# Kernel optimization log

Hardware: AMD Instinct MI355X
Metric: run time of the kernel (lower is better)

The kernel has to match this reference:

```python
import jax, jax.numpy as jnp
import numpy as np

# Static module configuration (matches init_kwargs)
B, C_IN, H, W = 128, 64, 32, 32
C_OUT = 128
K = 3
PAD = 1
STRIDE = 1
OUT_H = (H + 2 * PAD - K) // STRIDE + 1  # 32
OUT_W = (W + 2 * PAD - K) // STRIDE + 1  # 32
L = OUT_H * OUT_W                        # 1024
IN_FEAT = C_IN * K * K                   # 576


def setup_inputs() -> dict:
    key = jax.random.key(0)
    k1, k2, k3 = jax.random.split(key, 3)
    x = jax.random.normal(k1, (B, C_IN, H, W), dtype=jnp.float32)
    # kaiming-uniform-ish scale: 1/sqrt(fan_in)
    bound = 1.0 / np.sqrt(IN_FEAT)
    weight = jax.random.uniform(k2, (L, IN_FEAT, C_OUT), dtype=jnp.float32,
                                minval=-bound, maxval=bound)
    bias = jax.random.uniform(k3, (L, C_OUT), dtype=jnp.float32,
                              minval=-bound, maxval=bound)
    return {"x": x, "weight": weight, "bias": bias}


def _unfold(x):
    """torch.nn.Unfold equivalent: returns (B, L, C*K*K), channel-major feature order."""
    xp = jnp.pad(x, ((0, 0), (0, 0), (PAD, PAD), (PAD, PAD)))
    cols = []
    for i in range(K):
        for j in range(K):
            cols.append(xp[:, :, i:i + OUT_H * STRIDE:STRIDE,
                               j:j + OUT_W * STRIDE:STRIDE])
    # (B, C, K*K, out_h, out_w) -> feature index = c*K*K + i*K + j (torch unfold order)
    p = jnp.stack(cols, axis=2)
    p = p.reshape(x.shape[0], C_IN * K * K, L)
    return p.transpose(0, 2, 1)  # (B, L, in_feat)


def reference(x, weight, bias):
    patches = _unfold(x)                                  # (B, L, in_feat)
    out = jnp.einsum('bli,lio->blo', patches, weight)     # per-location matmul
    out = out + bias[None]                                # (B, L, out_ch)
    out = out.transpose(0, 2, 1).reshape(x.shape[0], C_OUT, OUT_H, OUT_W)
    out = jax.nn.relu(out)
    # MaxPool2d(2, 2)
    Bn = out.shape[0]
    out = out.reshape(Bn, C_OUT, OUT_H // 2, 2, OUT_W // 2, 2).max(axis=(3, 5))
    return out
```

## Files before the change

kernel.cpp:

```cpp
#include <hip/hip_runtime.h>

#define BB   128
#define CI   64
#define HH   32
#define WW   32
#define CO   128
#define IF   576
#define OW   32
#define XH   34
#define XW   34
#define XP_CB    (CI*BB)
#define XP_ELEMS ((size_t)XH*XW*CI*BB)
#define BK   32
#define NIT  72
#define LDK  40
#define COB  64

using short8 = __attribute__((ext_vector_type(8))) short;
using bf16x4 = __attribute__((ext_vector_type(4))) short;
using f32x4  = __attribute__((ext_vector_type(4))) float;

__device__ __forceinline__ unsigned short f2bf(float f) {
  union { float f; unsigned int u; } v; v.f = f;
  unsigned int u = v.u;
  u = (u + 0x7FFFu + ((u >> 16) & 1u)) >> 16;
  return (unsigned short)u;
}

__global__ __launch_bounds__(256) void transpose_x(
    const float* __restrict__ x, unsigned short* __restrict__ xp) {
  const int c = blockIdx.x >> 5;
  const int h = blockIdx.x & 31;
  __shared__ __align__(16) unsigned short tile[32][136];
  const int t = threadIdx.x;
  const int w = t & 31, b0 = t >> 5;
#pragma unroll
  for (int p = 0; p < 16; ++p) {
    int b = b0 + p * 8;
    float v = x[(((size_t)b * CI + c) * HH + h) * WW + w];
    tile[w][b] = f2bf(v);
  }
  __syncthreads();
  const int w2 = t >> 3;
  const int bb = (t & 7) * 16;
  const unsigned short* src = &tile[w2][bb];
  unsigned short* dst = xp + ((size_t)(h + 1) * XW + (w2 + 1)) * XP_CB + c * BB + bb;
  *(uint4*)(dst)     = *(const uint4*)(src);
  *(uint4*)(dst + 8) = *(const uint4*)(src + 8);
}

__global__ __launch_bounds__(512, 4) void local_gemm_pool(
    const float* __restrict__ Wt, const float* __restrict__ bias,
    const unsigned short* __restrict__ xp, float* __restrict__ out) {
  __shared__ __align__(16) unsigned short Asl[2][BB][LDK];
  __shared__ __align__(16) unsigned short Bsl[2][COB][LDK];
  __shared__ int offs[IF];

  const int tid  = threadIdx.x;
  const int lane = tid & 63;
  const int wave = tid >> 6;

  for (int kk = tid; kk < IF; kk += 512) {
    int c = kk / 9, r = kk % 9, di = r / 3, dj = r % 3;
    offs[kk] = ((di * XW + dj) * CI + c) * BB;
  }

  const int bidx = blockIdx.x;
  const int x8 = bidx & 7, j = bidx >> 3;
  const int coh = j & 1;
  const int pw  = (j >> 1) & 15;
  const int ph  = 2 * x8 + (j >> 5);
  const int co0 = coh * COB;

  const int sa = tid & 127;
  const int ka = tid >> 7;
  const int sb = tid & 63;
  const int kb = tid >> 6;

  const int r16 = lane & 15;
  const int q8  = (lane >> 4) * 8;
  const int m0  = (wave >> 2) * 64;
  const int n0  = (wave & 3) * 16;

  f32x4 acc[4] = {};
  f32x4 rmx[4] = {};

  float          breg0[4], breg1[4];
  unsigned short areg0[8], areg1[8];

  __syncthreads();

  auto issue = [&](int it, float* br, unsigned short* ar) {
    const int loc = it / 18, kc = it % 18, k0 = kc * BK;
    const int oh = 2 * ph + (loc >> 1), ow = 2 * pw + (loc & 1);
    const int l  = oh * OW + ow;
    const float* wp = Wt + ((size_t)l * IF + (k0 + kb * 4)) * CO + co0 + sb;
#pragma unroll
    for (int i = 0; i < 4; ++i) br[i] = wp[(size_t)i * CO];
    const int base = (oh * XW + ow) * XP_CB + sa;
#pragma unroll
    for (int i = 0; i < 8; ++i) ar[i] = xp[base + offs[k0 + ka * 8 + i]];
  };

  auto writeLds = [&](int it, const float* br, const unsigned short* ar) {
    const int bufI = it & 1;
    bf16x4 vb;
#pragma unroll
    for (int i = 0; i < 4; ++i) vb[i] = (short)f2bf(br[i]);
    *(bf16x4*)&Bsl[bufI][sb][kb * 4] = vb;
    short8 va;
#pragma unroll
    for (int i = 0; i < 8; ++i) va[i] = (short)ar[i];
    *(short8*)&Asl[bufI][sa][ka * 8] = va;
  };

  auto computeChunk = [&](int it) {
    const int bufI = it & 1;
    short8 af[4], bf;
#pragma unroll
    for (int tm = 0; tm < 4; ++tm)
      af[tm] = *(const short8*)&Asl[bufI][m0 + tm * 16 + r16][q8];
    bf = *(const short8*)&Bsl[bufI][n0 + r16][q8];
#pragma unroll
    for (int tm = 0; tm < 4; ++tm)
      acc[tm] = __builtin_amdgcn_mfma_f32_16x16x32_bf16(af[tm], bf, acc[tm], 0, 0, 0);
  };

  auto finishLoc = [&](int loc) {
    const int oh = 2 * ph + (loc >> 1), ow = 2 * pw + (loc & 1);
    const int l  = oh * OW + ow;
    const float bv = bias[l * CO + co0 + n0 + r16];
#pragma unroll
    for (int tm = 0; tm < 4; ++tm)
#pragma unroll
      for (int e = 0; e < 4; ++e) {
        float v = acc[tm][e] + bv;
        v = v > 0.f ? v : 0.f;
        rmx[tm][e] = fmaxf(rmx[tm][e], v);
        acc[tm][e] = 0.f;
      }
  };

  issue(0, breg0, areg0);
  issue(1, breg1, areg1);
  writeLds(0, breg0, areg0);
  __syncthreads();

  for (int it2 = 0; it2 < NIT; it2 += 2) {
    if (it2 + 2 < NIT) issue(it2 + 2, breg0, areg0);
    computeChunk(it2);
    writeLds(it2 + 1, breg1, areg1);
    __syncthreads();
    const int ito = it2 + 1;
    if (ito + 2 < NIT) issue(ito + 2, breg1, areg1);
    computeChunk(ito);
    if (ito + 1 < NIT) writeLds(ito + 1, breg0, areg0);
    if (ito % 18 == 17) finishLoc(ito / 18);
    __syncthreads();
  }

  float* op = out + (ph * 16 + pw);
  const int col = co0 + n0 + r16;
#pragma unroll
  for (int tm = 0; tm < 4; ++tm)
#pragma unroll
    for (int e = 0; e < 4; ++e) {
      const int row = m0 + tm * 16 + (lane >> 4) * 4 + e;
      op[((size_t)row * CO + col) * 256] = rmx[tm][e];
    }
}

extern "C" void kernel_launch(void* const* d_in, const int* in_sizes, int n_in,
                              void* d_out, int out_size, void* d_ws, size_t ws_size,
                              hipStream_t stream) {
  (void)in_sizes; (void)n_in; (void)out_size; (void)ws_size;
  const float* x  = (const float*)d_in[0];
  const float* w  = (const float*)d_in[1];
  const float* bs = (const float*)d_in[2];
  float* out = (float*)d_out;
  unsigned short* xp = (unsigned short*)d_ws;

  hipMemsetAsync(xp, 0, XP_ELEMS * sizeof(unsigned short), stream);
  transpose_x<<<dim3(CI * HH), dim3(256), 0, stream>>>(x, xp);
  local_gemm_pool<<<dim3(512), dim3(512), 0, stream>>>(w, bs, xp, out);
}
```

Measured before the change: 460.8 us.

## Reorder K loop by kernel tap, fuse halo zeroing, use packed bf16 convert

The reduction is reordered so each 32-wide chunk covers one (di,dj) tap and 32 channels. Activation gathers become strided loads without the LDS offset table, and weight rows are read with a stride of 9. The full memset of the padded buffer is dropped; the transpose kernel now zeroes only the halo border. Weight conversion to bf16 uses the packed v_cvt_pk_bf16_f32 instruction, which is round-to-nearest and should match the old manual rounding. Weight reads are now strided across feature rows, which may hurt coalescing per issue.

```diff
diff --git a/kernel.cpp b/kernel.cpp
--- a/kernel.cpp
+++ b/kernel.cpp
@@ -17,7 +17,6 @@
 #define COB  64
 
 using short8 = __attribute__((ext_vector_type(8))) short;
-using bf16x4 = __attribute__((ext_vector_type(4))) short;
 using f32x4  = __attribute__((ext_vector_type(4))) float;
 
 __device__ __forceinline__ unsigned short f2bf(float f) {
@@ -25,6 +24,12 @@
   unsigned int u = v.u;
   u = (u + 0x7FFFu + ((u >> 16) & 1u)) >> 16;
   return (unsigned short)u;
+}
+
+__device__ __forceinline__ unsigned int cvt_pk_bf16(float lo, float hi) {
+  unsigned int r;
+  asm("v_cvt_pk_bf16_f32 %0, %1, %2" : "=v"(r) : "v"(lo), "v"(hi));
+  return r;
 }
 
 __global__ __launch_bounds__(256) void transpose_x(
@@ -47,6 +52,17 @@
   unsigned short* dst = xp + ((size_t)(h + 1) * XW + (w2 + 1)) * XP_CB + c * BB + bb;
   *(uint4*)(dst)     = *(const uint4*)(src);
   *(uint4*)(dst + 8) = *(const uint4*)(src + 8);
+
+  if (blockIdx.x < 132) {
+    int s = blockIdx.x, hh, wh;
+    if (s < 34)      { hh = 0;  wh = s; }
+    else if (s < 68) { hh = 33; wh = s - 34; }
+    else             { int k = s - 68; hh = 1 + (k >> 1); wh = (k & 1) * 33; }
+    uint4 z; z.x = z.y = z.z = z.w = 0u;
+    uint4* p = (uint4*)(xp + ((size_t)hh * XW + wh) * XP_CB) + t;
+#pragma unroll
+    for (int q = 0; q < 4; ++q) p[q * 256] = z;
+  }
 }
 
 __global__ __launch_bounds__(512, 4) void local_gemm_pool(
@@ -54,16 +70,10 @@
     const unsigned short* __restrict__ xp, float* __restrict__ out) {
   __shared__ __align__(16) unsigned short Asl[2][BB][LDK];
   __shared__ __align__(16) unsigned short Bsl[2][COB][LDK];
-  __shared__ int offs[IF];
 
   const int tid  = threadIdx.x;
   const int lane = tid & 63;
   const int wave = tid >> 6;
-
-  for (int kk = tid; kk < IF; kk += 512) {
-    int c = kk / 9, r = kk % 9, di = r / 3, dj = r % 3;
-    offs[kk] = ((di * XW + dj) * CI + c) * BB;
-  }
 
   const int bidx = blockIdx.x;
   const int x8 = bidx & 7, j = bidx >> 3;
@@ -88,26 +98,28 @@
   float          breg0[4], breg1[4];
   unsigned short areg0[8], areg1[8];
 
-  __syncthreads();
-
   auto issue = [&](int it, float* br, unsigned short* ar) {
-    const int loc = it / 18, kc = it % 18, k0 = kc * BK;
+    const int loc = it / 18, kc = it % 18;
+    const int r = kc >> 1, c0 = (kc & 1) * 32;
+    const int di = r / 3, dj = r % 3;
     const int oh = 2 * ph + (loc >> 1), ow = 2 * pw + (loc & 1);
     const int l  = oh * OW + ow;
-    const float* wp = Wt + ((size_t)l * IF + (k0 + kb * 4)) * CO + co0 + sb;
+    const float* wp = Wt + ((size_t)l * IF + (size_t)(c0 + kb * 4) * 9 + r) * CO
+                         + co0 + sb;
 #pragma unroll
-    for (int i = 0; i < 4; ++i) br[i] = wp[(size_t)i * CO];
-    const int base = (oh * XW + ow) * XP_CB + sa;
+    for (int i = 0; i < 4; ++i) br[i] = wp[(size_t)i * 9 * CO];
+    const unsigned short* ap = xp + ((size_t)(oh + di) * XW + (ow + dj)) * XP_CB
+                                  + (c0 + ka * 8) * BB + sa;
 #pragma unroll
-    for (int i = 0; i < 8; ++i) ar[i] = xp[base + offs[k0 + ka * 8 + i]];
+    for (int i = 0; i < 8; ++i) ar[i] = ap[i * BB];
   };
 
   auto writeLds = [&](int it, const float* br, const unsigned short* ar) {
     const int bufI = it & 1;
-    bf16x4 vb;
-#pragma unroll
-    for (int i = 0; i < 4; ++i) vb[i] = (short)f2bf(br[i]);
-    *(bf16x4*)&Bsl[bufI][sb][kb * 4] = vb;
+    uint2 vb;
+    vb.x = cvt_pk_bf16(br[0], br[1]);
+    vb.y = cvt_pk_bf16(br[2], br[3]);
+    *(uint2*)&Bsl[bufI][sb][kb * 4] = vb;
     short8 va;
 #pragma unroll
     for (int i = 0; i < 8; ++i) va[i] = (short)ar[i];
@@ -180,7 +192,6 @@
   float* out = (float*)d_out;
   unsigned short* xp = (unsigned short*)d_ws;
 
-  hipMemsetAsync(xp, 0, XP_ELEMS * sizeof(unsigned short), stream);
   transpose_x<<<dim3(CI * HH), dim3(256), 0, stream>>>(x, xp);
   local_gemm_pool<<<dim3(512), dim3(512), 0, stream>>>(w, bs, xp, out);
 }
```

Measured after the change: 460.3 us. No clear change (-0.1%).
